# Kernel optimization log

Hardware: AMD Instinct MI355X
Metric: run time of the kernel (lower is better)

## Reference

```python
import jax, jax.numpy as jnp
import numpy as np

B, T, C, H = 4, 2048, 1024, 16
HD = C // H


def setup_inputs() -> dict:
    key = jax.random.key(0)
    ks = jax.random.split(key, 5)
    s = 1.0 / np.sqrt(C)
    return {
        "x": jax.random.normal(ks[0], (B, T, C), dtype=jnp.float32),
        "Wq": jax.random.normal(ks[1], (C, C), dtype=jnp.float32) * s,
        "bq": jnp.zeros((C,), dtype=jnp.float32),
        "Wk": jax.random.normal(ks[2], (C, C), dtype=jnp.float32) * s,
        "bk": jnp.zeros((C,), dtype=jnp.float32),
        "Wv": jax.random.normal(ks[3], (C, C), dtype=jnp.float32) * s,
        "bv": jnp.zeros((C,), dtype=jnp.float32),
        "Wp": jax.random.normal(ks[4], (C, C), dtype=jnp.float32) * s,
        "bp": jnp.zeros((C,), dtype=jnp.float32),
    }


def reference(x, Wq, bq, Wk, bk, Wv, bv, Wp, bp):
    Bs, Ts, Cs = x.shape
    # projections (Linear applies x @ W^T + b; W here stored as [out,in])
    q = (x @ Wq.T + bq).reshape(Bs, Ts, H, HD).transpose(0, 2, 1, 3)  # [B,H,T,hd]
    k = (x @ Wk.T + bk).reshape(Bs, Ts, H, HD).transpose(0, 2, 1, 3)
    v = (x @ Wv.T + bv).reshape(Bs, Ts, H, HD).transpose(0, 2, 1, 3)
    scale = 1.0 / jnp.sqrt(jnp.asarray(HD, dtype=x.dtype))
    att = jnp.einsum("bhqd,bhkd->bhqk", q, k) * scale  # [B,H,T,T]
    causal = jnp.tril(jnp.ones((Ts, Ts), dtype=bool))
    att = jnp.where(causal[None, None], att, jnp.asarray(-jnp.inf, dtype=att.dtype))
    att = jax.nn.softmax(att, axis=-1)
    # dropout: DROPOUT constant undefined in source; eval mode -> identity
    y = jnp.einsum("bhqk,bhkd->bhqd", att, v)  # [B,H,T,hd]
    y = y.transpose(0, 2, 1, 3).reshape(Bs, Ts, Cs)
    return y @ Wp.T + bp
```

## Files before the change

### kernel.cpp

```cpp
#include <hip/hip_runtime.h>
#include <hip/hip_bf16.h>


using bf16   = __bf16;
using bf16x8 = __attribute__((ext_vector_type(8))) __bf16;
using bf16x4 = __attribute__((ext_vector_type(4))) __bf16;
using f32x4  = __attribute__((ext_vector_type(4))) float;

#define MFMA16(a, b, c) __builtin_amdgcn_mfma_f32_16x16x32_bf16((a), (b), (c), 0, 0, 0)

__global__ __launch_bounds__(256) void qkv_gemm(
    const float* __restrict__ x,
    const float* __restrict__ Wq, const float* __restrict__ Wk, const float* __restrict__ Wv,
    const float* __restrict__ bq, const float* __restrict__ bk, const float* __restrict__ bv,
    bf16* __restrict__ qws, bf16* __restrict__ kws, bf16* __restrict__ vws)
{
    __shared__ bf16 As[128][72];
    __shared__ bf16 Bs[128][72];
    const int tid  = threadIdx.x;
    const int lane = tid & 63;
    const int wid  = tid >> 6;
    const int bm   = blockIdx.x;
    const int bn   = blockIdx.y;
    const int widx  = bn >> 3;
    const int nbase = (bn & 7) << 7;
    const float* __restrict__ W    = (widx == 0) ? Wq : (widx == 1) ? Wk : Wv;
    const float* __restrict__ bias = (widx == 0) ? bq : (widx == 1) ? bk : bv;
    bf16* __restrict__ outp        = (widx == 0) ? qws : (widx == 1) ? kws : vws;

    const int wr   = (wid >> 1) << 6;
    const int wc   = (wid & 1) << 6;
    const int lr16 = lane & 15;
    const int lk8  = (lane >> 4) << 3;

    f32x4 acc[4][4];
#pragma unroll
    for (int m = 0; m < 4; ++m)
#pragma unroll
        for (int n = 0; n < 4; ++n)
            acc[m][n] = (f32x4){0.f, 0.f, 0.f, 0.f};

    for (int kt = 0; kt < 16; ++kt) {
        const int k0 = kt << 6;
        __syncthreads();
#pragma unroll
        for (int i = 0; i < 8; ++i) {
            const int f   = tid + (i << 8);
            const int row = f >> 4;
            const int c4  = (f & 15) << 2;
            const float4 v = *(const float4*)(x + (size_t)(bm * 128 + row) * 1024 + k0 + c4);
            bf16x4 pk = {(bf16)v.x, (bf16)v.y, (bf16)v.z, (bf16)v.w};
            *(bf16x4*)(&As[row][c4]) = pk;
        }
#pragma unroll
        for (int i = 0; i < 8; ++i) {
            const int f   = tid + (i << 8);
            const int row = f >> 4;
            const int c4  = (f & 15) << 2;
            const float4 v = *(const float4*)(W + (size_t)(nbase + row) * 1024 + k0 + c4);
            bf16x4 pk = {(bf16)v.x, (bf16)v.y, (bf16)v.z, (bf16)v.w};
            *(bf16x4*)(&Bs[row][c4]) = pk;
        }
        __syncthreads();
#pragma unroll
        for (int ks = 0; ks < 2; ++ks) {
            bf16x8 af[4], bfr[4];
#pragma unroll
            for (int m = 0; m < 4; ++m)
                af[m] = *(const bf16x8*)(&As[wr + m * 16 + lr16][ks * 32 + lk8]);
#pragma unroll
            for (int n = 0; n < 4; ++n)
                bfr[n] = *(const bf16x8*)(&Bs[wc + n * 16 + lr16][ks * 32 + lk8]);
#pragma unroll
            for (int m = 0; m < 4; ++m)
#pragma unroll
                for (int n = 0; n < 4; ++n)
                    acc[m][n] = MFMA16(af[m], bfr[n], acc[m][n]);
        }
    }

    const int r4 = (lane >> 4) << 2;
#pragma unroll
    for (int n = 0; n < 4; ++n) {
        const int ncol = nbase + wc + n * 16 + lr16;
        const float bia = bias[ncol];
        const int h = ncol >> 6, d = ncol & 63;
#pragma unroll
        for (int m = 0; m < 4; ++m) {
#pragma unroll
            for (int r = 0; r < 4; ++r) {
                const int grow = bm * 128 + wr + m * 16 + r4 + r;
                const int b = grow >> 11, t = grow & 2047;
                outp[((size_t)(b * 16 + h) * 2048 + t) * 64 + d] = (bf16)(acc[m][n][r] + bia);
            }
        }
    }
}

__global__ __launch_bounds__(256) void vtrans(const bf16* __restrict__ v, bf16* __restrict__ vt)
{
    __shared__ bf16 Ts[64][72];
    const int tid = threadIdx.x;
    const int bh  = blockIdx.y;
    const int t0  = blockIdx.x << 6;
#pragma unroll
    for (int i = 0; i < 2; ++i) {
        const int c   = tid + (i << 8);
        const int row = c >> 3;
        const int c8  = (c & 7) << 3;
        *(bf16x8*)(&Ts[row][c8]) = *(const bf16x8*)(v + ((size_t)bh * 2048 + t0 + row) * 64 + c8);
    }
    __syncthreads();
#pragma unroll
    for (int i = 0; i < 2; ++i) {
        const int c    = tid + (i << 8);
        const int drow = c >> 3;
        const int t8   = (c & 7) << 3;
        bf16x8 o;
#pragma unroll
        for (int j = 0; j < 8; ++j) o[j] = Ts[t8 + j][drow];
        *(bf16x8*)(vt + ((size_t)bh * 64 + drow) * 2048 + t0 + t8) = o;
    }
}

__global__ __launch_bounds__(256, 2) void attn_kernel(
    const bf16* __restrict__ q, const bf16* __restrict__ k,
    const bf16* __restrict__ vt, bf16* __restrict__ y)
{
    __shared__ bf16 Ks[2][64][72];
    __shared__ bf16 Vs[2][64][72];
    __shared__ bf16 Ps[4][32][72];
    const int tid  = threadIdx.x;
    const int lane = tid & 63;
    const int wid  = tid >> 6;
    const int lin  = blockIdx.x;
    const int xcd  = lin & 7;
    const int jj   = lin >> 3;
    const int bh   = xcd + ((jj >> 3) << 3);
    const int pr   = jj & 7;
    const int bb   = bh >> 4, hh = bh & 15;
    const bf16* __restrict__ qp  = q  + (size_t)bh * 2048 * 64;
    const bf16* __restrict__ kp  = k  + (size_t)bh * 2048 * 64;
    const bf16* __restrict__ vtp = vt + (size_t)bh * 64 * 2048;
    const int lr16 = lane & 15;
    const int lk8  = (lane >> 4) << 3;
    const int r4   = (lane >> 4) << 2;
    const float SCL = 0.18033688f;
    const int srow = tid >> 3;
    const int scol = (tid & 7) << 3;

    for (int half = 0; half < 2; ++half) {
        const int s    = half ? (15 - pr) : pr;
        const int q0   = s << 7;
        const int nt   = 2 * s + 2;
        const int wrow = q0 + wid * 32;

        bf16x8 qf[2][2];
#pragma unroll
        for (int mi = 0; mi < 2; ++mi)
#pragma unroll
            for (int dk = 0; dk < 2; ++dk)
                qf[mi][dk] = *(const bf16x8*)(qp + (size_t)(wrow + mi * 16 + lr16) * 64 + dk * 32 + lk8);

        f32x4 of[2][4];
        float mS[2][4], lp[2][4];
#pragma unroll
        for (int mi = 0; mi < 2; ++mi)
#pragma unroll
            for (int nf = 0; nf < 4; ++nf) of[mi][nf] = (f32x4){0.f, 0.f, 0.f, 0.f};
#pragma unroll
        for (int mi = 0; mi < 2; ++mi)
#pragma unroll
            for (int r = 0; r < 4; ++r) { mS[mi][r] = -1e30f; lp[mi][r] = 0.f; }

        {
            bf16x8 ka = *(const bf16x8*)(kp + (size_t)srow * 64 + scol);
            bf16x8 kb = *(const bf16x8*)(kp + (size_t)(srow + 32) * 64 + scol);
            bf16x8 va = *(const bf16x8*)(vtp + (size_t)srow * 2048 + scol);
            bf16x8 vb = *(const bf16x8*)(vtp + (size_t)(srow + 32) * 2048 + scol);
            *(bf16x8*)(&Ks[0][srow][scol])      = ka;
            *(bf16x8*)(&Ks[0][srow + 32][scol]) = kb;
            *(bf16x8*)(&Vs[0][srow][scol])      = va;
            *(bf16x8*)(&Vs[0][srow + 32][scol]) = vb;
        }
        int cur = 0;

        for (int t = 0; t < nt; ++t) {
            const int kv0 = t << 6;
            __syncthreads();
            bf16x8 ka, kb, va, vb;
            const bool pf = (t + 1 < nt);
            if (pf) {
                const int kn = kv0 + 64;
                ka = *(const bf16x8*)(kp + (size_t)(kn + srow) * 64 + scol);
                kb = *(const bf16x8*)(kp + (size_t)(kn + srow + 32) * 64 + scol);
                va = *(const bf16x8*)(vtp + (size_t)srow * 2048 + kn + scol);
                vb = *(const bf16x8*)(vtp + (size_t)(srow + 32) * 2048 + kn + scol);
            }
            f32x4 sv[2][4];
#pragma unroll
            for (int mi = 0; mi < 2; ++mi)
#pragma unroll
                for (int kf = 0; kf < 4; ++kf)
                    sv[mi][kf] = (f32x4){0.f, 0.f, 0.f, 0.f};
#pragma unroll
            for (int kf = 0; kf < 4; ++kf) {
                const bf16x8 k0 = *(const bf16x8*)(&Ks[cur][kf * 16 + lr16][lk8]);
                const bf16x8 k1 = *(const bf16x8*)(&Ks[cur][kf * 16 + lr16][32 + lk8]);
                sv[0][kf] = MFMA16(qf[0][0], k0, sv[0][kf]);
                sv[0][kf] = MFMA16(qf[0][1], k1, sv[0][kf]);
                sv[1][kf] = MFMA16(qf[1][0], k0, sv[1][kf]);
                sv[1][kf] = MFMA16(qf[1][1], k1, sv[1][kf]);
            }
#pragma unroll
            for (int mi = 0; mi < 2; ++mi) {
                const int rb = wrow + mi * 16;
                if (kv0 + 63 > rb) {
#pragma unroll
                    for (int kf = 0; kf < 4; ++kf) {
                        const int kk = kv0 + kf * 16 + lr16;
#pragma unroll
                        for (int r = 0; r < 4; ++r)
                            if (kk > rb + r4 + r) sv[mi][kf][r] = -3.0e38f;
                    }
                }
            }
            float gmax[2][4];
#pragma unroll
            for (int mi = 0; mi < 2; ++mi)
#pragma unroll
                for (int r = 0; r < 4; ++r) {
                    float g = fmaxf(fmaxf(sv[mi][0][r], sv[mi][1][r]),
                                    fmaxf(sv[mi][2][r], sv[mi][3][r]));
                    g = fmaxf(g, __shfl_xor(g, 1));
                    g = fmaxf(g, __shfl_xor(g, 2));
                    g = fmaxf(g, __shfl_xor(g, 4));
                    g = fmaxf(g, __shfl_xor(g, 8));
                    gmax[mi][r] = g;
                }
            bool needre = false;
#pragma unroll
            for (int mi = 0; mi < 2; ++mi)
#pragma unroll
                for (int r = 0; r < 4; ++r) needre |= (gmax[mi][r] > mS[mi][r] + 64.0f);
            if (__ballot(needre) != 0ull) {
#pragma unroll
                for (int mi = 0; mi < 2; ++mi)
#pragma unroll
                    for (int r = 0; r < 4; ++r) {
                        const float mn   = fmaxf(mS[mi][r], gmax[mi][r]);
                        const float corr = exp2f((mS[mi][r] - mn) * SCL);
                        mS[mi][r] = mn;
                        lp[mi][r] *= corr;
#pragma unroll
                        for (int nf = 0; nf < 4; ++nf) of[mi][nf][r] *= corr;
                    }
            }
#pragma unroll
            for (int mi = 0; mi < 2; ++mi) {
#pragma unroll
                for (int kf = 0; kf < 4; ++kf)
#pragma unroll
                    for (int r = 0; r < 4; ++r)
                        sv[mi][kf][r] = exp2f((sv[mi][kf][r] - mS[mi][r]) * SCL);
#pragma unroll
                for (int r = 0; r < 4; ++r)
                    lp[mi][r] += sv[mi][0][r] + sv[mi][1][r] + sv[mi][2][r] + sv[mi][3][r];
            }
#pragma unroll
            for (int mi = 0; mi < 2; ++mi)
#pragma unroll
                for (int kf = 0; kf < 4; ++kf)
#pragma unroll
                    for (int r = 0; r < 4; ++r)
                        Ps[wid][mi * 16 + r4 + r][kf * 16 + lr16] = (bf16)sv[mi][kf][r];
            asm volatile("s_waitcnt lgkmcnt(0)" ::: "memory");
            __builtin_amdgcn_sched_barrier(0);
            bf16x8 pa[2][2];
#pragma unroll
            for (int mi = 0; mi < 2; ++mi)
#pragma unroll
                for (int ks = 0; ks < 2; ++ks)
                    pa[mi][ks] = *(const bf16x8*)(&Ps[wid][mi * 16 + lr16][ks * 32 + lk8]);
#pragma unroll
            for (int nf = 0; nf < 4; ++nf) {
                const bf16x8 v0 = *(const bf16x8*)(&Vs[cur][nf * 16 + lr16][lk8]);
                const bf16x8 v1 = *(const bf16x8*)(&Vs[cur][nf * 16 + lr16][32 + lk8]);
                of[0][nf] = MFMA16(pa[0][0], v0, of[0][nf]);
                of[0][nf] = MFMA16(pa[0][1], v1, of[0][nf]);
                of[1][nf] = MFMA16(pa[1][0], v0, of[1][nf]);
                of[1][nf] = MFMA16(pa[1][1], v1, of[1][nf]);
            }
            if (pf) {
                *(bf16x8*)(&Ks[cur ^ 1][srow][scol])      = ka;
                *(bf16x8*)(&Ks[cur ^ 1][srow + 32][scol]) = kb;
                *(bf16x8*)(&Vs[cur ^ 1][srow][scol])      = va;
                *(bf16x8*)(&Vs[cur ^ 1][srow + 32][scol]) = vb;
            }
            cur ^= 1;
        }

#pragma unroll
        for (int mi = 0; mi < 2; ++mi)
#pragma unroll
            for (int r = 0; r < 4; ++r) {
                float l = lp[mi][r];
                l += __shfl_xor(l, 1);
                l += __shfl_xor(l, 2);
                l += __shfl_xor(l, 4);
                l += __shfl_xor(l, 8);
                lp[mi][r] = 1.0f / l;
            }
#pragma unroll
        for (int mi = 0; mi < 2; ++mi)
#pragma unroll
            for (int nf = 0; nf < 4; ++nf)
#pragma unroll
                for (int r = 0; r < 4; ++r)
                    y[((size_t)(bb * 2048 + wrow + mi * 16 + r4 + r)) * 1024 + hh * 64 + nf * 16 + lr16] =
                        (bf16)(of[mi][nf][r] * lp[mi][r]);
    }
}

__global__ __launch_bounds__(256) void out_gemm(
    const bf16* __restrict__ y, const float* __restrict__ Wp,
    const float* __restrict__ bp, float* __restrict__ out)
{
    __shared__ bf16 As[128][72];
    __shared__ bf16 Bs[128][72];
    const int tid  = threadIdx.x;
    const int lane = tid & 63;
    const int wid  = tid >> 6;
    const int bm   = blockIdx.x;
    const int nbase = blockIdx.y << 7;
    const int wr   = (wid >> 1) << 6;
    const int wc   = (wid & 1) << 6;
    const int lr16 = lane & 15;
    const int lk8  = (lane >> 4) << 3;

    f32x4 acc[4][4];
#pragma unroll
    for (int m = 0; m < 4; ++m)
#pragma unroll
        for (int n = 0; n < 4; ++n)
            acc[m][n] = (f32x4){0.f, 0.f, 0.f, 0.f};

    for (int kt = 0; kt < 16; ++kt) {
        const int k0 = kt << 6;
        __syncthreads();
#pragma unroll
        for (int i = 0; i < 4; ++i) {
            const int c   = tid + (i << 8);
            const int row = c >> 3;
            const int c8  = (c & 7) << 3;
            *(bf16x8*)(&As[row][c8]) = *(const bf16x8*)(y + (size_t)(bm * 128 + row) * 1024 + k0 + c8);
        }
#pragma unroll
        for (int i = 0; i < 8; ++i) {
            const int f   = tid + (i << 8);
            const int row = f >> 4;
            const int c4  = (f & 15) << 2;
            const float4 v = *(const float4*)(Wp + (size_t)(nbase + row) * 1024 + k0 + c4);
            bf16x4 pk = {(bf16)v.x, (bf16)v.y, (bf16)v.z, (bf16)v.w};
            *(bf16x4*)(&Bs[row][c4]) = pk;
        }
        __syncthreads();
#pragma unroll
        for (int ks = 0; ks < 2; ++ks) {
            bf16x8 af[4], bfr[4];
#pragma unroll
            for (int m = 0; m < 4; ++m)
                af[m] = *(const bf16x8*)(&As[wr + m * 16 + lr16][ks * 32 + lk8]);
#pragma unroll
            for (int n = 0; n < 4; ++n)
                bfr[n] = *(const bf16x8*)(&Bs[wc + n * 16 + lr16][ks * 32 + lk8]);
#pragma unroll
            for (int m = 0; m < 4; ++m)
#pragma unroll
                for (int n = 0; n < 4; ++n)
                    acc[m][n] = MFMA16(af[m], bfr[n], acc[m][n]);
        }
    }

    const int r4 = (lane >> 4) << 2;
#pragma unroll
    for (int n = 0; n < 4; ++n) {
        const int ncol = nbase + wc + n * 16 + lr16;
        const float bia = bp[ncol];
#pragma unroll
        for (int m = 0; m < 4; ++m) {
#pragma unroll
            for (int r = 0; r < 4; ++r) {
                const int grow = bm * 128 + wr + m * 16 + r4 + r;
                out[(size_t)grow * 1024 + ncol] = acc[m][n][r] + bia;
            }
        }
    }
}

extern "C" void kernel_launch(void* const* d_in, const int* in_sizes, int n_in,
                              void* d_out, int out_size, void* d_ws, size_t ws_size,
                              hipStream_t stream) {
    const float* x  = (const float*)d_in[0];
    const float* Wq = (const float*)d_in[1];
    const float* bq = (const float*)d_in[2];
    const float* Wk = (const float*)d_in[3];
    const float* bk = (const float*)d_in[4];
    const float* Wv = (const float*)d_in[5];
    const float* bv = (const float*)d_in[6];
    const float* Wp = (const float*)d_in[7];
    const float* bp = (const float*)d_in[8];
    float* out = (float*)d_out;

    char* ws = (char*)d_ws;
    const size_t MB16 = (size_t)16 * 1024 * 1024;
    bf16* qws  = (bf16*)(ws);
    bf16* kws  = (bf16*)(ws + MB16);
    bf16* vws  = (bf16*)(ws + 2 * MB16);
    bf16* vtws = (bf16*)(ws + 3 * MB16);
    bf16* yws  = vws;

    qkv_gemm<<<dim3(64, 24), 256, 0, stream>>>(x, Wq, Wk, Wv, bq, bk, bv, qws, kws, vws);
    vtrans<<<dim3(32, 64), 256, 0, stream>>>(vws, vtws);
    attn_kernel<<<512, 256, 0, stream>>>(qws, kws, vtws, yws);
    out_gemm<<<dim3(64, 8), 256, 0, stream>>>(yws, Wp, bp, out);
}
```

Measured before the change: 333.7 us.

## Pre-convert inputs to bf16, use direct global-to-LDS loads, transpose attention MFMAs

Adds kernels that convert x, the QKV weights and Wp to bf16 once, staging them in the output buffer and workspace. Both GEMMs then load tiles with global_load_lds instead of converting fp32 in registers. The QKV GEMM writes V already transposed, so the separate vtrans kernel is removed. Attention is rewritten in transposed form (K·Q and V·P) so that max and row-sum reductions need fewer shuffles, and the row sum is computed with an MFMA against a ones vector. In exchange it adds extra launches and conversion traffic, and the unpadded LDS tiles may cause bank conflicts.

```diff
diff --git a/kernel.cpp b/kernel.cpp
--- a/kernel.cpp
+++ b/kernel.cpp
@@ -9,30 +9,77 @@
 
 #define MFMA16(a, b, c) __builtin_amdgcn_mfma_f32_16x16x32_bf16((a), (b), (c), 0, 0, 0)
 
+__device__ __forceinline__ void gll16(const bf16* g, bf16* l) {
+    __builtin_amdgcn_global_load_lds(
+        (const __attribute__((address_space(1))) void*)(g),
+        (__attribute__((address_space(3))) void*)(l),
+        16, 0, 0);
+}
+
+__device__ __forceinline__ unsigned cvtpk(float lo, float hi) {
+    unsigned r;
+    asm("v_cvt_pk_bf16_f32 %0, %1, %2" : "=v"(r) : "v"(lo), "v"(hi));
+    return r;
+}
+
+__global__ __launch_bounds__(256) void conv_xw(
+    const float* __restrict__ x, const float* __restrict__ Wq,
+    const float* __restrict__ Wk, const float* __restrict__ Wv,
+    bf16* __restrict__ xb, bf16* __restrict__ wb)
+{
+    const int n = 2883584;
+    for (int i = blockIdx.x * 256 + threadIdx.x; i < n; i += gridDim.x * 256) {
+        const float* src; bf16* dst; int off;
+        if (i < 2097152) { src = x; dst = xb; off = i; }
+        else {
+            const int j = i - 2097152;
+            const int w = j >> 18;
+            off = j & 262143;
+            src = (w == 0) ? Wq : (w == 1) ? Wk : Wv;
+            dst = wb + ((size_t)w << 20);
+        }
+        const float4 v = *(const float4*)(src + (size_t)off * 4);
+        bf16x4 pk = {(bf16)v.x, (bf16)v.y, (bf16)v.z, (bf16)v.w};
+        *(bf16x4*)(dst + (size_t)off * 4) = pk;
+    }
+}
+
+__global__ __launch_bounds__(256) void conv_wp(const float* __restrict__ Wp,
+                                               bf16* __restrict__ wpb)
+{
+    const int n = 262144;
+    for (int i = blockIdx.x * 256 + threadIdx.x; i < n; i += gridDim.x * 256) {
+        const float4 v = *(const float4*)(Wp + (size_t)i * 4);
+        bf16x4 pk = {(bf16)v.x, (bf16)v.y, (bf16)v.z, (bf16)v.w};
+        *(bf16x4*)(wpb + (size_t)i * 4) = pk;
+    }
+}
+
 __global__ __launch_bounds__(256) void qkv_gemm(
-    const float* __restrict__ x,
-    const float* __restrict__ Wq, const float* __restrict__ Wk, const float* __restrict__ Wv,
+    const bf16* __restrict__ xb, const bf16* __restrict__ wb,
     const float* __restrict__ bq, const float* __restrict__ bk, const float* __restrict__ bv,
-    bf16* __restrict__ qws, bf16* __restrict__ kws, bf16* __restrict__ vws)
+    bf16* __restrict__ qws, bf16* __restrict__ kws, bf16* __restrict__ vtws)
 {
-    __shared__ bf16 As[128][72];
-    __shared__ bf16 Bs[128][72];
+    __shared__ bf16 As[128][64];
+    __shared__ bf16 Bs[128][64];
     const int tid  = threadIdx.x;
     const int lane = tid & 63;
     const int wid  = tid >> 6;
     const int bm   = blockIdx.x;
     const int bn   = blockIdx.y;
-    const int widx  = bn >> 3;
-    const int nbase = (bn & 7) << 7;
-    const float* __restrict__ W    = (widx == 0) ? Wq : (widx == 1) ? Wk : Wv;
+    const int widx = bn >> 3;
     const float* __restrict__ bias = (widx == 0) ? bq : (widx == 1) ? bk : bv;
-    bf16* __restrict__ outp        = (widx == 0) ? qws : (widx == 1) ? kws : vws;
 
     const int wr   = (wid >> 1) << 6;
     const int wc   = (wid & 1) << 6;
     const int lr16 = lane & 15;
     const int lk8  = (lane >> 4) << 3;
 
+    const int lrow = lane >> 3;
+    const int lcol = (lane & 7) << 3;
+    const bf16* ga = xb + (size_t)(bm * 128 + wid * 32 + lrow) * 1024 + lcol;
+    const bf16* gb = wb + (size_t)(bn * 128 + wid * 32 + lrow) * 1024 + lcol;
+
     f32x4 acc[4][4];
 #pragma unroll
     for (int m = 0; m < 4; ++m)
@@ -44,23 +91,11 @@
         const int k0 = kt << 6;
         __syncthreads();
 #pragma unroll
-        for (int i = 0; i < 8; ++i) {
-            const int f   = tid + (i << 8);
-            const int row = f >> 4;
-            const int c4  = (f & 15) << 2;
-            const float4 v = *(const float4*)(x + (size_t)(bm * 128 + row) * 1024 + k0 + c4);
-            bf16x4 pk = {(bf16)v.x, (bf16)v.y, (bf16)v.z, (bf16)v.w};
-            *(bf16x4*)(&As[row][c4]) = pk;
-        }
-#pragma unroll
-        for (int i = 0; i < 8; ++i) {
-            const int f   = tid + (i << 8);
-            const int row = f >> 4;
-            const int c4  = (f & 15) << 2;
-            const float4 v = *(const float4*)(W + (size_t)(nbase + row) * 1024 + k0 + c4);
-            bf16x4 pk = {(bf16)v.x, (bf16)v.y, (bf16)v.z, (bf16)v.w};
-            *(bf16x4*)(&Bs[row][c4]) = pk;
-        }
+        for (int i = 0; i < 4; ++i) {
+            gll16(ga + (size_t)i * 8192 + k0, &As[wid * 32 + i * 8][0]);
+            gll16(gb + (size_t)i * 8192 + k0, &Bs[wid * 32 + i * 8][0]);
+        }
+        asm volatile("s_waitcnt vmcnt(0)" ::: "memory");
         __syncthreads();
 #pragma unroll
         for (int ks = 0; ks < 2; ++ks) {
@@ -82,44 +117,25 @@
     const int r4 = (lane >> 4) << 2;
 #pragma unroll
     for (int n = 0; n < 4; ++n) {
-        const int ncol = nbase + wc + n * 16 + lr16;
-        const float bia = bias[ncol];
-        const int h = ncol >> 6, d = ncol & 63;
+        const int ncol = bn * 128 + wc + n * 16 + lr16;
+        const int c10  = ncol & 1023;
+        const float bia = bias[c10];
+        const int h = c10 >> 6, d = c10 & 63;
 #pragma unroll
         for (int m = 0; m < 4; ++m) {
 #pragma unroll
             for (int r = 0; r < 4; ++r) {
                 const int grow = bm * 128 + wr + m * 16 + r4 + r;
                 const int b = grow >> 11, t = grow & 2047;
-                outp[((size_t)(b * 16 + h) * 2048 + t) * 64 + d] = (bf16)(acc[m][n][r] + bia);
-            }
-        }
-    }
-}
-
-__global__ __launch_bounds__(256) void vtrans(const bf16* __restrict__ v, bf16* __restrict__ vt)
-{
-    __shared__ bf16 Ts[64][72];
-    const int tid = threadIdx.x;
-    const int bh  = blockIdx.y;
-    const int t0  = blockIdx.x << 6;
-#pragma unroll
-    for (int i = 0; i < 2; ++i) {
-        const int c   = tid + (i << 8);
-        const int row = c >> 3;
-        const int c8  = (c & 7) << 3;
-        *(bf16x8*)(&Ts[row][c8]) = *(const bf16x8*)(v + ((size_t)bh * 2048 + t0 + row) * 64 + c8);
-    }
-    __syncthreads();
-#pragma unroll
-    for (int i = 0; i < 2; ++i) {
-        const int c    = tid + (i << 8);
-        const int drow = c >> 3;
-        const int t8   = (c & 7) << 3;
-        bf16x8 o;
-#pragma unroll
-        for (int j = 0; j < 8; ++j) o[j] = Ts[t8 + j][drow];
-        *(bf16x8*)(vt + ((size_t)bh * 64 + drow) * 2048 + t0 + t8) = o;
+                const bf16 val = (bf16)(acc[m][n][r] + bia);
+                if (widx == 2)
+                    vtws[((size_t)(b * 16 + h) * 64 + d) * 2048 + t] = val;
+                else if (widx == 0)
+                    qws[((size_t)(b * 16 + h) * 2048 + t) * 64 + d] = val;
+                else
+                    kws[((size_t)(b * 16 + h) * 2048 + t) * 64 + d] = val;
+            }
+        }
     }
 }
 
@@ -143,11 +159,14 @@
     const bf16* __restrict__ kp  = k  + (size_t)bh * 2048 * 64;
     const bf16* __restrict__ vtp = vt + (size_t)bh * 64 * 2048;
     const int lr16 = lane & 15;
-    const int lk8  = (lane >> 4) << 3;
-    const int r4   = (lane >> 4) << 2;
+    const int g    = lane >> 4;
+    const int lk8  = g << 3;
+    const int r4   = g << 2;
     const float SCL = 0.18033688f;
     const int srow = tid >> 3;
     const int scol = (tid & 7) << 3;
+    const bf16 one = (bf16)1.0f;
+    const bf16x8 onesf = {one, one, one, one, one, one, one, one};
 
     for (int half = 0; half < 2; ++half) {
         const int s    = half ? (15 - pr) : pr;
@@ -162,16 +181,16 @@
             for (int dk = 0; dk < 2; ++dk)
                 qf[mi][dk] = *(const bf16x8*)(qp + (size_t)(wrow + mi * 16 + lr16) * 64 + dk * 32 + lk8);
 
-        f32x4 of[2][4];
-        float mS[2][4], lp[2][4];
-#pragma unroll
-        for (int mi = 0; mi < 2; ++mi)
-#pragma unroll
-            for (int nf = 0; nf < 4; ++nf) of[mi][nf] = (f32x4){0.f, 0.f, 0.f, 0.f};
-#pragma unroll
-        for (int mi = 0; mi < 2; ++mi)
-#pragma unroll
-            for (int r = 0; r < 4; ++r) { mS[mi][r] = -1e30f; lp[mi][r] = 0.f; }
+        f32x4 ofT[2][4];
+        f32x4 lsum[2];
+        float mS[2];
+#pragma unroll
+        for (int mi = 0; mi < 2; ++mi) {
+            lsum[mi] = (f32x4){0.f, 0.f, 0.f, 0.f};
+            mS[mi]   = -1e30f;
+#pragma unroll
+            for (int df = 0; df < 4; ++df) ofT[mi][df] = (f32x4){0.f, 0.f, 0.f, 0.f};
+        }
 
         {
             bf16x8 ka = *(const bf16x8*)(kp + (size_t)srow * 64 + scol);
@@ -197,100 +216,90 @@
                 va = *(const bf16x8*)(vtp + (size_t)srow * 2048 + kn + scol);
                 vb = *(const bf16x8*)(vtp + (size_t)(srow + 32) * 2048 + kn + scol);
             }
-            f32x4 sv[2][4];
-#pragma unroll
-            for (int mi = 0; mi < 2; ++mi)
-#pragma unroll
-                for (int kf = 0; kf < 4; ++kf)
-                    sv[mi][kf] = (f32x4){0.f, 0.f, 0.f, 0.f};
+            const f32x4 z = (f32x4){0.f, 0.f, 0.f, 0.f};
+            f32x4 sT[2][4];
 #pragma unroll
             for (int kf = 0; kf < 4; ++kf) {
-                const bf16x8 k0 = *(const bf16x8*)(&Ks[cur][kf * 16 + lr16][lk8]);
-                const bf16x8 k1 = *(const bf16x8*)(&Ks[cur][kf * 16 + lr16][32 + lk8]);
-                sv[0][kf] = MFMA16(qf[0][0], k0, sv[0][kf]);
-                sv[0][kf] = MFMA16(qf[0][1], k1, sv[0][kf]);
-                sv[1][kf] = MFMA16(qf[1][0], k0, sv[1][kf]);
-                sv[1][kf] = MFMA16(qf[1][1], k1, sv[1][kf]);
+                const bf16x8 k0f = *(const bf16x8*)(&Ks[cur][kf * 16 + lr16][lk8]);
+                const bf16x8 k1f = *(const bf16x8*)(&Ks[cur][kf * 16 + lr16][32 + lk8]);
+                sT[0][kf] = MFMA16(k1f, qf[0][1], MFMA16(k0f, qf[0][0], z));
+                sT[1][kf] = MFMA16(k1f, qf[1][1], MFMA16(k0f, qf[1][0], z));
             }
 #pragma unroll
             for (int mi = 0; mi < 2; ++mi) {
-                const int rb = wrow + mi * 16;
-                if (kv0 + 63 > rb) {
+                if (kv0 + 63 > wrow + mi * 16) {
+                    const int qq = wrow + mi * 16 + lr16;
 #pragma unroll
                     for (int kf = 0; kf < 4; ++kf) {
-                        const int kk = kv0 + kf * 16 + lr16;
+                        const int kkb = kv0 + kf * 16 + r4;
 #pragma unroll
                         for (int r = 0; r < 4; ++r)
-                            if (kk > rb + r4 + r) sv[mi][kf][r] = -3.0e38f;
+                            if (kkb + r > qq) sT[mi][kf][r] = -3.0e38f;
                     }
                 }
             }
-            float gmax[2][4];
+            float gmax[2];
+#pragma unroll
+            for (int mi = 0; mi < 2; ++mi) {
+                float a = fmaxf(fmaxf(sT[mi][0][0], sT[mi][0][1]), fmaxf(sT[mi][0][2], sT[mi][0][3]));
+                float b = fmaxf(fmaxf(sT[mi][1][0], sT[mi][1][1]), fmaxf(sT[mi][1][2], sT[mi][1][3]));
+                float c = fmaxf(fmaxf(sT[mi][2][0], sT[mi][2][1]), fmaxf(sT[mi][2][2], sT[mi][2][3]));
+                float d = fmaxf(fmaxf(sT[mi][3][0], sT[mi][3][1]), fmaxf(sT[mi][3][2], sT[mi][3][3]));
+                float m = fmaxf(fmaxf(a, b), fmaxf(c, d));
+                m = fmaxf(m, __shfl_xor(m, 16));
+                m = fmaxf(m, __shfl_xor(m, 32));
+                gmax[mi] = m;
+            }
+            const bool needre = (gmax[0] > mS[0] + 64.0f) | (gmax[1] > mS[1] + 64.0f);
+            if (__ballot(needre) != 0ull) {
+#pragma unroll
+                for (int mi = 0; mi < 2; ++mi) {
+                    const float mn   = fmaxf(mS[mi], gmax[mi]);
+                    const float corr = exp2f((mS[mi] - mn) * SCL);
+                    mS[mi] = mn;
+                    lsum[mi][0] *= corr;
+#pragma unroll
+                    for (int df = 0; df < 4; ++df) ofT[mi][df] *= corr;
+                }
+            }
 #pragma unroll
             for (int mi = 0; mi < 2; ++mi)
 #pragma unroll
-                for (int r = 0; r < 4; ++r) {
-                    float g = fmaxf(fmaxf(sv[mi][0][r], sv[mi][1][r]),
-                                    fmaxf(sv[mi][2][r], sv[mi][3][r]));
-                    g = fmaxf(g, __shfl_xor(g, 1));
-                    g = fmaxf(g, __shfl_xor(g, 2));
-                    g = fmaxf(g, __shfl_xor(g, 4));
-                    g = fmaxf(g, __shfl_xor(g, 8));
-                    gmax[mi][r] = g;
+                for (int kf = 0; kf < 4; ++kf)
+#pragma unroll
+                    for (int r = 0; r < 4; ++r)
+                        sT[mi][kf][r] = exp2f((sT[mi][kf][r] - mS[mi]) * SCL);
+#pragma unroll
+            for (int mi = 0; mi < 2; ++mi) {
+#pragma unroll
+                for (int kf = 0; kf < 4; ++kf) {
+                    uint2 u;
+                    u.x = cvtpk(sT[mi][kf][0], sT[mi][kf][1]);
+                    u.y = cvtpk(sT[mi][kf][2], sT[mi][kf][3]);
+                    *(uint2*)(&Ps[wid][mi * 16 + lr16][kf * 16 + r4]) = u;
                 }
-            bool needre = false;
-#pragma unroll
-            for (int mi = 0; mi < 2; ++mi)
-#pragma unroll
-                for (int r = 0; r < 4; ++r) needre |= (gmax[mi][r] > mS[mi][r] + 64.0f);
-            if (__ballot(needre) != 0ull) {
-#pragma unroll
-                for (int mi = 0; mi < 2; ++mi)
-#pragma unroll
-                    for (int r = 0; r < 4; ++r) {
-                        const float mn   = fmaxf(mS[mi][r], gmax[mi][r]);
-                        const float corr = exp2f((mS[mi][r] - mn) * SCL);
-                        mS[mi][r] = mn;
-                        lp[mi][r] *= corr;
-#pragma unroll
-                        for (int nf = 0; nf < 4; ++nf) of[mi][nf][r] *= corr;
-                    }
-            }
-#pragma unroll
-            for (int mi = 0; mi < 2; ++mi) {
-#pragma unroll
-                for (int kf = 0; kf < 4; ++kf)
-#pragma unroll
-                    for (int r = 0; r < 4; ++r)
-                        sv[mi][kf][r] = exp2f((sv[mi][kf][r] - mS[mi][r]) * SCL);
-#pragma unroll
-                for (int r = 0; r < 4; ++r)
-                    lp[mi][r] += sv[mi][0][r] + sv[mi][1][r] + sv[mi][2][r] + sv[mi][3][r];
-            }
-#pragma unroll
-            for (int mi = 0; mi < 2; ++mi)
-#pragma unroll
-                for (int kf = 0; kf < 4; ++kf)
-#pragma unroll
-                    for (int r = 0; r < 4; ++r)
-                        Ps[wid][mi * 16 + r4 + r][kf * 16 + lr16] = (bf16)sv[mi][kf][r];
+            }
             asm volatile("s_waitcnt lgkmcnt(0)" ::: "memory");
             __builtin_amdgcn_sched_barrier(0);
-            bf16x8 pa[2][2];
+            bf16x8 pb[2][2];
 #pragma unroll
             for (int mi = 0; mi < 2; ++mi)
 #pragma unroll
                 for (int ks = 0; ks < 2; ++ks)
-                    pa[mi][ks] = *(const bf16x8*)(&Ps[wid][mi * 16 + lr16][ks * 32 + lk8]);
-#pragma unroll
-            for (int nf = 0; nf < 4; ++nf) {
-                const bf16x8 v0 = *(const bf16x8*)(&Vs[cur][nf * 16 + lr16][lk8]);
-                const bf16x8 v1 = *(const bf16x8*)(&Vs[cur][nf * 16 + lr16][32 + lk8]);
-                of[0][nf] = MFMA16(pa[0][0], v0, of[0][nf]);
-                of[0][nf] = MFMA16(pa[0][1], v1, of[0][nf]);
-                of[1][nf] = MFMA16(pa[1][0], v0, of[1][nf]);
-                of[1][nf] = MFMA16(pa[1][1], v1, of[1][nf]);
-            }
+                    pb[mi][ks] = *(const bf16x8*)(&Ps[wid][mi * 16 + lr16][ks * 32 + lk8]);
+#pragma unroll
+            for (int df = 0; df < 4; ++df) {
+                const bf16x8 v0 = *(const bf16x8*)(&Vs[cur][df * 16 + lr16][lk8]);
+                const bf16x8 v1 = *(const bf16x8*)(&Vs[cur][df * 16 + lr16][32 + lk8]);
+                ofT[0][df] = MFMA16(v0, pb[0][0], ofT[0][df]);
+                ofT[0][df] = MFMA16(v1, pb[0][1], ofT[0][df]);
+                ofT[1][df] = MFMA16(v0, pb[1][0], ofT[1][df]);
+                ofT[1][df] = MFMA16(v1, pb[1][1], ofT[1][df]);
+            }
+            lsum[0] = MFMA16(onesf, pb[0][0], lsum[0]);
+            lsum[0] = MFMA16(onesf, pb[0][1], lsum[0]);
+            lsum[1] = MFMA16(onesf, pb[1][0], lsum[1]);
+            lsum[1] = MFMA16(onesf, pb[1][1], lsum[1]);
             if (pf) {
                 *(bf16x8*)(&Ks[cur ^ 1][srow][scol])      = ka;
                 *(bf16x8*)(&Ks[cur ^ 1][srow + 32][scol]) = kb;
@@ -301,42 +310,37 @@
         }
 
 #pragma unroll
-        for (int mi = 0; mi < 2; ++mi)
-#pragma unroll
-            for (int r = 0; r < 4; ++r) {
-                float l = lp[mi][r];
-                l += __shfl_xor(l, 1);
-                l += __shfl_xor(l, 2);
-                l += __shfl_xor(l, 4);
-                l += __shfl_xor(l, 8);
-                lp[mi][r] = 1.0f / l;
-            }
-#pragma unroll
-        for (int mi = 0; mi < 2; ++mi)
-#pragma unroll
-            for (int nf = 0; nf < 4; ++nf)
+        for (int mi = 0; mi < 2; ++mi) {
+            const float linv = 1.0f / lsum[mi][0];
+            const size_t rowb = ((size_t)(bb * 2048 + wrow + mi * 16 + lr16)) * 1024 + hh * 64;
+#pragma unroll
+            for (int df = 0; df < 4; ++df)
 #pragma unroll
                 for (int r = 0; r < 4; ++r)
-                    y[((size_t)(bb * 2048 + wrow + mi * 16 + r4 + r)) * 1024 + hh * 64 + nf * 16 + lr16] =
-                        (bf16)(of[mi][nf][r] * lp[mi][r]);
+                    y[rowb + df * 16 + r4 + r] = (bf16)(ofT[mi][df][r] * linv);
+        }
     }
 }
 
 __global__ __launch_bounds__(256) void out_gemm(
-    const bf16* __restrict__ y, const float* __restrict__ Wp,
+    const bf16* __restrict__ y, const bf16* __restrict__ wpb,
     const float* __restrict__ bp, float* __restrict__ out)
 {
-    __shared__ bf16 As[128][72];
-    __shared__ bf16 Bs[128][72];
+    __shared__ bf16 As[128][64];
+    __shared__ bf16 Bs[128][64];
     const int tid  = threadIdx.x;
     const int lane = tid & 63;
     const int wid  = tid >> 6;
     const int bm   = blockIdx.x;
-    const int nbase = blockIdx.y << 7;
+    const int bn   = blockIdx.y;
     const int wr   = (wid >> 1) << 6;
     const int wc   = (wid & 1) << 6;
     const int lr16 = lane & 15;
     const int lk8  = (lane >> 4) << 3;
+    const int lrow = lane >> 3;
+    const int lcol = (lane & 7) << 3;
+    const bf16* ga = y   + (size_t)(bm * 128 + wid * 32 + lrow) * 1024 + lcol;
+    const bf16* gb = wpb + (size_t)(bn * 128 + wid * 32 + lrow) * 1024 + lcol;
 
     f32x4 acc[4][4];
 #pragma unroll
@@ -350,20 +354,10 @@
         __syncthreads();
 #pragma unroll
         for (int i = 0; i < 4; ++i) {
-            const int c   = tid + (i << 8);
-            const int row = c >> 3;
-            const int c8  = (c & 7) << 3;
-            *(bf16x8*)(&As[row][c8]) = *(const bf16x8*)(y + (size_t)(bm * 128 + row) * 1024 + k0 + c8);
-        }
-#pragma unroll
-        for (int i = 0; i < 8; ++i) {
-            const int f   = tid + (i << 8);
-            const int row = f >> 4;
-            const int c4  = (f & 15) << 2;
-            const float4 v = *(const float4*)(Wp + (size_t)(nbase + row) * 1024 + k0 + c4);
-            bf16x4 pk = {(bf16)v.x, (bf16)v.y, (bf16)v.z, (bf16)v.w};
-            *(bf16x4*)(&Bs[row][c4]) = pk;
-        }
+            gll16(ga + (size_t)i * 8192 + k0, &As[wid * 32 + i * 8][0]);
+            gll16(gb + (size_t)i * 8192 + k0, &Bs[wid * 32 + i * 8][0]);
+        }
+        asm volatile("s_waitcnt vmcnt(0)" ::: "memory");
         __syncthreads();
 #pragma unroll
         for (int ks = 0; ks < 2; ++ks) {
@@ -385,7 +379,7 @@
     const int r4 = (lane >> 4) << 2;
 #pragma unroll
     for (int n = 0; n < 4; ++n) {
-        const int ncol = nbase + wc + n * 16 + lr16;
+        const int ncol = bn * 128 + wc + n * 16 + lr16;
         const float bia = bp[ncol];
 #pragma unroll
         for (int m = 0; m < 4; ++m) {
@@ -416,12 +410,17 @@
     const size_t MB16 = (size_t)16 * 1024 * 1024;
     bf16* qws  = (bf16*)(ws);
     bf16* kws  = (bf16*)(ws + MB16);
-    bf16* vws  = (bf16*)(ws + 2 * MB16);
-    bf16* vtws = (bf16*)(ws + 3 * MB16);
-    bf16* yws  = vws;
-
-    qkv_gemm<<<dim3(64, 24), 256, 0, stream>>>(x, Wq, Wk, Wv, bq, bk, bv, qws, kws, vws);
-    vtrans<<<dim3(32, 64), 256, 0, stream>>>(vws, vtws);
+    bf16* vtws = (bf16*)(ws + 2 * MB16);
+    bf16* yws  = (bf16*)(ws + 3 * MB16);
+    bf16* wpb  = kws;
+
+    char* ob = (char*)d_out;
+    bf16* xb = (bf16*)(ob);
+    bf16* wb = (bf16*)(ob + MB16);
+
+    conv_xw<<<2048, 256, 0, stream>>>(x, Wq, Wk, Wv, xb, wb);
+    qkv_gemm<<<dim3(64, 24), 256, 0, stream>>>(xb, wb, bq, bk, bv, qws, kws, vtws);
     attn_kernel<<<512, 256, 0, stream>>>(qws, kws, vtws, yws);
-    out_gemm<<<dim3(64, 8), 256, 0, stream>>>(yws, Wp, bp, out);
-}
+    conv_wp<<<256, 256, 0, stream>>>(Wp, wpb);
+    out_gemm<<<dim3(64, 8), 256, 0, stream>>>(yws, wpb, bp, out);
+}
```

After: 291.9 us. 12.5% less time.
